# Performance work log

Hardware: AMD Instinct MI355X
Metric: run time of the kernel (lower is better)

Reference implementation:

```python
import jax, jax.numpy as jnp
import numpy as np

N_NODES = 50000


def gcn_conv(x, W, b, src, dst, n):
    # PyG GCNConv: linear transform, add self-loops, symmetric normalization,
    # scatter-add aggregation from src -> dst, then bias.
    h = x @ W  # [N, out]
    loop = jnp.arange(n, dtype=src.dtype)
    s = jnp.concatenate([src, loop])
    d = jnp.concatenate([dst, loop])
    deg = jax.ops.segment_sum(jnp.ones(s.shape[0], dtype=h.dtype), d, num_segments=n)
    dinv = jnp.where(deg > 0, jax.lax.rsqrt(deg), 0.0)
    norm = dinv[s] * dinv[d]  # [E+N]
    msg = h[s] * norm[:, None]
    out = jax.ops.segment_sum(msg, d, num_segments=n)
    return out + b


def setup_inputs() -> dict:
    key = jax.random.key(0)
    ks = jax.random.split(key, 10)
    F_in, H, C = 256, 128, 128
    E, EL = 320000, 200000
    x = jax.random.normal(ks[0], (N_NODES, F_in), dtype=jnp.float32)
    edge_index = jax.random.randint(ks[1], (2, E), 0, N_NODES, dtype=jnp.int32)
    edge_label_index = jax.random.randint(ks[2], (2, EL), 0, N_NODES, dtype=jnp.int32)
    def glorot(k, shape):
        lim = np.sqrt(6.0 / (shape[0] + shape[1]))
        return jax.random.uniform(k, shape, jnp.float32, -lim, lim)
    W0 = glorot(ks[3], (F_in, H))
    b0 = jnp.zeros((H,), jnp.float32)
    W1 = glorot(ks[4], (H, H))
    b1 = jnp.zeros((H,), jnp.float32)
    W2 = glorot(ks[5], (H, C))
    b2 = jnp.zeros((C,), jnp.float32)
    return {"x": x, "edge_index": edge_index, "edge_label_index": edge_label_index,
            "W0": W0, "b0": b0, "W1": W1, "b1": b1, "W2": W2, "b2": b2}


def reference(x, edge_index, edge_label_index, W0, b0, W1, b1, W2, b2):
    src, dst = edge_index[0], edge_index[1]
    n = x.shape[0]
    # drop_edge keep_ratio == 1.0 -> all edges kept (deterministic)
    h = jax.nn.relu(gcn_conv(x, W0, b0, src, dst, n))
    h = jax.nn.relu(gcn_conv(h, W1, b1, src, dst, n))
    z = gcn_conv(h, W2, b2, src, dst, n)  # final conv, no activation
    # decode: dot product over candidate edge pairs
    eli = edge_label_index.astype(jnp.int32)
    logits = jnp.sum(z[eli[0]] * z[eli[1]], axis=-1)  # [E_label]
    return logits
```

## Files before the change

kernel.cpp:

```cpp
#include <hip/hip_runtime.h>
#include <hip/hip_bf16.h>


typedef __attribute__((ext_vector_type(8))) short short8v;
typedef __attribute__((ext_vector_type(4))) float f32x4;

__device__ inline unsigned bf16_rne(float f) {
    unsigned u = __float_as_uint(f);
    return (u + 0x7FFF + ((u >> 16) & 1)) >> 16;
}


__global__ void count_deg_kernel(const int* __restrict__ dst, int* __restrict__ deg, int E) {
    int e = blockIdx.x * blockDim.x + threadIdx.x;
    if (e < E) atomicAdd(&deg[dst[e]], 1);
}

__global__ __launch_bounds__(1024) void scan1_kernel(int* __restrict__ data,
                                                     int* __restrict__ sums, int n) {
    __shared__ int tmp[1024];
    int t = threadIdx.x;
    int idx = blockIdx.x * 1024 + t;
    int val = (idx < n) ? data[idx] : 0;
    tmp[t] = val;
    __syncthreads();
#pragma unroll
    for (int off = 1; off < 1024; off <<= 1) {
        int v = (t >= off) ? tmp[t - off] : 0;
        __syncthreads();
        tmp[t] += v;
        __syncthreads();
    }
    if (idx < n) data[idx] = tmp[t] - val;
    if (t == 1023) sums[blockIdx.x] = tmp[t];
}

__global__ void scan2_kernel(int* __restrict__ sums, int nb) {
    int lane = threadIdx.x & 63;
    int v = (lane < nb) ? sums[lane] : 0;
    int orig = v;
#pragma unroll
    for (int d = 1; d < 64; d <<= 1) {
        int t2 = __shfl_up(v, d, 64);
        if (lane >= d) v += t2;
    }
    if (lane < nb) sums[lane] = v - orig;
}

__global__ __launch_bounds__(1024) void scan3_kernel(int* __restrict__ data,
                                                     const int* __restrict__ sums, int n) {
    int idx = blockIdx.x * 1024 + threadIdx.x;
    if (idx < n && blockIdx.x > 0) data[idx] += sums[blockIdx.x];
}

__global__ void make_dinv_kernel(const int* __restrict__ off, float* __restrict__ dinv,
                                 int n, int E) {
    int v = blockIdx.x * blockDim.x + threadIdx.x;
    if (v < n) {
        int o1 = (v + 1 < n) ? off[v + 1] : E;
        float d = (float)(o1 - off[v]) + 1.0f;
        dinv[v] = 1.0f / sqrtf(d);
    }
}

__global__ void csr_fill_kernel(const int* __restrict__ src, const int* __restrict__ dst,
                                const int* __restrict__ off, int* __restrict__ fill,
                                int* __restrict__ csr_src, int E) {
    int e = blockIdx.x * blockDim.x + threadIdx.x;
    if (e >= E) return;
    int d = dst[e];
    int pos = atomicAdd(&fill[d], 1);
    csr_src[off[d] + pos] = src[e];
}


__global__ void split_w_kernel(const float* __restrict__ W, short* __restrict__ Whp,
                               short* __restrict__ Wlp, int K) {
    int idx = blockIdx.x * blockDim.x + threadIdx.x;
    if (idx >= K * 128) return;
    int k = idx >> 7, col = idx & 127;
    float f = W[idx];
    unsigned h = bf16_rne(f);
    float fh = __uint_as_float(h << 16);
    unsigned l = bf16_rne(f - fh);
    int NS = K >> 5;
    int c = col >> 4, col16 = col & 15, s = k >> 5, q = (k >> 3) & 3, j = k & 7;
    int waddr = (c * NS + s) * 512 + q * 128 + col16 * 8 + j;
    Whp[waddr] = (short)h;
    Wlp[waddr] = (short)l;
}


template<int K>
__global__ __launch_bounds__(256) void pack_a_kernel(const float* __restrict__ x,
                                                     short* __restrict__ Ahp,
                                                     short* __restrict__ Alp,
                                                     int M, int ntiles) {
    int gid = blockIdx.x * blockDim.x + threadIdx.x;
    const int CH = K / 8;
    if (gid >= ntiles * 16 * CH) return;
    int r  = gid & 15;
    int c8 = (gid >> 4) % CH;
    int g  = gid / (16 * CH);
    int row = g * 16 + r;
    if (row >= M) row = M - 1;
    const float* xp = x + (size_t)row * K + c8 * 8;
    float4 v0 = *reinterpret_cast<const float4*>(xp);
    float4 v1 = *reinterpret_cast<const float4*>(xp + 4);
    float f[8] = {v0.x, v0.y, v0.z, v0.w, v1.x, v1.y, v1.z, v1.w};
    short8v hv, lv;
#pragma unroll
    for (int j = 0; j < 8; ++j) {
        unsigned h = bf16_rne(f[j]);
        float fh = __uint_as_float(h << 16);
        unsigned l = bf16_rne(f[j] - fh);
        hv[j] = (short)h;
        lv[j] = (short)l;
    }
    size_t waddr = (size_t)g * 16 * K + c8 * 128 + r * 8;
    *reinterpret_cast<short8v*>(&Ahp[waddr]) = hv;
    *reinterpret_cast<short8v*>(&Alp[waddr]) = lv;
}


template<int K>
__global__ __launch_bounds__(256) void gemm_mfma_packed(const short* __restrict__ Ahp,
                                                        const short* __restrict__ Alp,
                                                        const short* __restrict__ Whp,
                                                        const short* __restrict__ Wlp,
                                                        const float* __restrict__ dinv,
                                                        float* __restrict__ out,
                                                        int M) {
    constexpr int NS = K / 32;
    const int lane = threadIdx.x & 63;
    const int w = threadIdx.x >> 6;
    const int gtile = blockIdx.x * 4 + w;
    const int row16 = gtile * 16;
    if (row16 >= M) return;

    const short* ab = Ahp + (size_t)gtile * 16 * K + lane * 8;
    const short* lb = Alp + (size_t)gtile * 16 * K + lane * 8;

    short8v ah[NS], al[NS];
#pragma unroll
    for (int s = 0; s < NS; ++s) {
        ah[s] = *reinterpret_cast<const short8v*>(ab + s * 512);
        al[s] = *reinterpret_cast<const short8v*>(lb + s * 512);
    }

    f32x4 acc[8];
#pragma unroll
    for (int c = 0; c < 8; ++c) acc[c] = (f32x4){0.f, 0.f, 0.f, 0.f};

#pragma unroll
    for (int c = 0; c < 8; ++c) {
        const short* bb = Whp + (size_t)(c * NS) * 512 + lane * 8;
        const short* cb = Wlp + (size_t)(c * NS) * 512 + lane * 8;
#pragma unroll
        for (int s = 0; s < NS; ++s) {
            short8v bh = *reinterpret_cast<const short8v*>(bb + s * 512);
            short8v bl = *reinterpret_cast<const short8v*>(cb + s * 512);
            acc[c] = __builtin_amdgcn_mfma_f32_16x16x32_bf16(ah[s], bh, acc[c], 0, 0, 0);
            acc[c] = __builtin_amdgcn_mfma_f32_16x16x32_bf16(ah[s], bl, acc[c], 0, 0, 0);
            acc[c] = __builtin_amdgcn_mfma_f32_16x16x32_bf16(al[s], bh, acc[c], 0, 0, 0);
        }
    }

#pragma unroll
    for (int r = 0; r < 4; ++r) {
        int row = row16 + (lane >> 4) * 4 + r;
        if (row < M) {
            float ds = dinv[row];
#pragma unroll
            for (int c = 0; c < 8; ++c)
                out[(size_t)row * 128 + c * 16 + (lane & 15)] = acc[c][r] * ds;
        }
    }
}


template<int PACKED>
__global__ __launch_bounds__(256) void gather_kernel(const int* __restrict__ off,
                                                     const int* __restrict__ csr_src,
                                                     const float* __restrict__ dinv,
                                                     const float* __restrict__ hp,
                                                     const float* __restrict__ bias,
                                                     float* __restrict__ outf,
                                                     short* __restrict__ Ahp,
                                                     short* __restrict__ Alp,
                                                     int n, int E, int do_relu) {
    int gid = blockIdx.x * blockDim.x + threadIdx.x;
    int v = gid >> 6;
    int lane = gid & 63;
    if (v >= n) return;

    int o0 = off[v];
    int o1 = (v + 1 < n) ? off[v + 1] : E;

    const float2* __restrict__ hp2 = reinterpret_cast<const float2*>(hp);
    float2 sv = hp2[(size_t)v * 64 + lane];
    float ax = sv.x, ay = sv.y;
    float bx = 0.0f, by = 0.0f;

    for (int base = o0; base < o1; base += 64) {
        int cnt = min(64, o1 - base);
        int myidx = (lane < cnt) ? csr_src[base + lane] : 0;
        int j = 0;
        for (; j + 4 <= cnt; j += 4) {
            int i0 = __shfl(myidx, j,     64);
            int i1 = __shfl(myidx, j + 1, 64);
            int i2 = __shfl(myidx, j + 2, 64);
            int i3 = __shfl(myidx, j + 3, 64);
            float2 h0 = hp2[(size_t)i0 * 64 + lane];
            float2 h1 = hp2[(size_t)i1 * 64 + lane];
            float2 h2 = hp2[(size_t)i2 * 64 + lane];
            float2 h3 = hp2[(size_t)i3 * 64 + lane];
            ax += h0.x; ay += h0.y;
            bx += h1.x; by += h1.y;
            ax += h2.x; ay += h2.y;
            bx += h3.x; by += h3.y;
        }
        for (; j < cnt; ++j) {
            int s = __shfl(myidx, j, 64);
            float2 hv = hp2[(size_t)s * 64 + lane];
            ax += hv.x; ay += hv.y;
        }
    }

    float dv = dinv[v];
    float2 bb = *reinterpret_cast<const float2*>(&bias[lane * 2]);
    float ox = dv * (ax + bx) + bb.x;
    float oy = dv * (ay + by) + bb.y;
    if (do_relu) { ox = fmaxf(ox, 0.0f); oy = fmaxf(oy, 0.0f); }

    if (PACKED) {
        unsigned h0 = bf16_rne(ox);
        unsigned l0 = bf16_rne(ox - __uint_as_float(h0 << 16));
        unsigned h1 = bf16_rne(oy);
        unsigned l1 = bf16_rne(oy - __uint_as_float(h1 << 16));
        int g = v >> 4, r = v & 15;
        int c8 = lane >> 2;
        int j0 = (2 * lane) & 7;
        size_t a = (size_t)g * 2048 + c8 * 128 + r * 8 + j0;
        short2 hv = make_short2((short)h0, (short)h1);
        short2 lv = make_short2((short)l0, (short)l1);
        *reinterpret_cast<short2*>(&Ahp[a]) = hv;
        *reinterpret_cast<short2*>(&Alp[a]) = lv;
    } else {
        *reinterpret_cast<float2*>(&outf[(size_t)v * 128 + lane * 2]) = make_float2(ox, oy);
    }
}


__global__ __launch_bounds__(256) void decode_kernel(const int* __restrict__ ia,
                                                     const int* __restrict__ ib,
                                                     const float* __restrict__ z,
                                                     float* __restrict__ out, int EL) {
    int gid = blockIdx.x * blockDim.x + threadIdx.x;
    int e = gid >> 5;
    int l5 = gid & 31;
    if (e >= EL) return;
    int a = ia[e], b = ib[e];
    const float4* z4 = reinterpret_cast<const float4*>(z);
    float4 za = z4[(size_t)a * 32 + l5];
    float4 zb = z4[(size_t)b * 32 + l5];
    float s = za.x * zb.x + za.y * zb.y + za.z * zb.z + za.w * zb.w;
#pragma unroll
    for (int off = 16; off > 0; off >>= 1) s += __shfl_down(s, off, 64);
    if (l5 == 0) out[e] = s;
}


extern "C" void kernel_launch(void* const* d_in, const int* in_sizes, int n_in,
                              void* d_out, int out_size, void* d_ws, size_t ws_size,
                              hipStream_t stream) {
    const float* x   = (const float*)d_in[0];
    const int*   ei  = (const int*)d_in[1];
    const int*   eli = (const int*)d_in[2];
    const float* W0  = (const float*)d_in[3];
    const float* b0  = (const float*)d_in[4];
    const float* W1  = (const float*)d_in[5];
    const float* b1  = (const float*)d_in[6];
    const float* W2  = (const float*)d_in[7];
    const float* b2  = (const float*)d_in[8];
    float* out = (float*)d_out;

    const int H    = in_sizes[4];
    const int F_in = in_sizes[3] / H;
    const int n    = in_sizes[0] / F_in;
    const int E    = in_sizes[1] / 2;
    const int EL   = in_sizes[2] / 2;

    const int* src = ei;
    const int* dst = ei + E;
    const int* la  = eli;
    const int* lb  = eli + EL;

    const int ntiles = (n + 15) / 16;

    char* ws = (char*)d_ws;
    size_t p = 0;
    auto alloc = [&](size_t bytes) { char* r = ws + p; p = (p + bytes + 255) & ~(size_t)255; return r; };
    float* dinv    = (float*)alloc((size_t)n * 4);
    int*   off     = (int*)  alloc((size_t)n * 4);
    int*   csr_src = (int*)  alloc((size_t)E * 4);
    int*   sums    = (int*)  alloc(64 * 4);
    short* W0h     = (short*)alloc((size_t)F_in * H * 2);
    short* W0l     = (short*)alloc((size_t)F_in * H * 2);
    short* W1h     = (short*)alloc((size_t)H * H * 2);
    short* W1l     = (short*)alloc((size_t)H * H * 2);
    short* W2h     = (short*)alloc((size_t)H * H * 2);
    short* W2l     = (short*)alloc((size_t)H * H * 2);
    short* pkh     = (short*)alloc((size_t)ntiles * 16 * F_in * 2);
    short* pkl     = (short*)alloc((size_t)ntiles * 16 * F_in * 2);
    float* bufA    = (float*)alloc((size_t)n * 128 * 4);
    float* bufB    = (float*)alloc((size_t)n * 128 * 4);
    int*   fill    = (int*)bufB;

    const int T = 256;
    dim3 blk(T);

    hipMemsetAsync(off, 0, (size_t)n * 4, stream);
    hipMemsetAsync(fill, 0, (size_t)n * 4, stream);
    split_w_kernel<<<(F_in * H + T - 1) / T, blk, 0, stream>>>(W0, W0h, W0l, F_in);
    split_w_kernel<<<(H * H + T - 1) / T, blk, 0, stream>>>(W1, W1h, W1l, H);
    split_w_kernel<<<(H * H + T - 1) / T, blk, 0, stream>>>(W2, W2h, W2l, H);
    {
        long long tot = (long long)ntiles * 16 * (F_in / 8);
        pack_a_kernel<256><<<(int)((tot + T - 1) / T), blk, 0, stream>>>(x, pkh, pkl, n, ntiles);
    }
    count_deg_kernel<<<(E + T - 1) / T, blk, 0, stream>>>(dst, off, E);
    int nb = (n + 1023) / 1024;
    scan1_kernel<<<nb, 1024, 0, stream>>>(off, sums, n);
    scan2_kernel<<<1, 64, 0, stream>>>(sums, nb);
    scan3_kernel<<<nb, 1024, 0, stream>>>(off, sums, n);
    make_dinv_kernel<<<(n + T - 1) / T, blk, 0, stream>>>(off, dinv, n, E);
    csr_fill_kernel<<<(E + T - 1) / T, blk, 0, stream>>>(src, dst, off, fill, csr_src, E);

    const int mblocks       = (ntiles + 3) / 4;
    const int gather_blocks = (int)(((long long)n * 64 + T - 1) / T);

    gemm_mfma_packed<256><<<mblocks, blk, 0, stream>>>(pkh, pkl, W0h, W0l, dinv, bufA, n);
    gather_kernel<1><<<gather_blocks, blk, 0, stream>>>(off, csr_src, dinv, bufA, b0,
                                                        nullptr, pkh, pkl, n, E, 1);

    gemm_mfma_packed<128><<<mblocks, blk, 0, stream>>>(pkh, pkl, W1h, W1l, dinv, bufA, n);
    gather_kernel<1><<<gather_blocks, blk, 0, stream>>>(off, csr_src, dinv, bufA, b1,
                                                        nullptr, pkh, pkl, n, E, 1);

    gemm_mfma_packed<128><<<mblocks, blk, 0, stream>>>(pkh, pkl, W2h, W2l, dinv, bufA, n);
    gather_kernel<0><<<gather_blocks, blk, 0, stream>>>(off, csr_src, dinv, bufA, b2,
                                                        bufB, nullptr, nullptr, n, E, 0);

    const int dec_blocks = (int)(((long long)EL * 32 + T - 1) / T);
    decode_kernel<<<dec_blocks, blk, 0, stream>>>(la, lb, bufB, out, EL);
}
```

Before: 338.1 us.

## Merge weight-split launches, unroll gather by eight, use 512-thread gather blocks

The three weight split-and-pack launches are merged into one kernel that selects the weight matrix by thread index, removing two launches. The gather kernel now runs 512-thread blocks holding 8 nodes each and adds an 8-way unrolled neighbor loop so more independent row loads are in flight. Average degree is about 7, so the 8-way path runs only for higher-degree nodes. Larger blocks may change occupancy and register use.

```diff
diff --git a/kernel.cpp b/kernel.cpp
--- a/kernel.cpp
+++ b/kernel.cpp
@@ -74,10 +74,8 @@
 }
 
 
-__global__ void split_w_kernel(const float* __restrict__ W, short* __restrict__ Whp,
-                               short* __restrict__ Wlp, int K) {
-    int idx = blockIdx.x * blockDim.x + threadIdx.x;
-    if (idx >= K * 128) return;
+__device__ inline void split_pack_one(const float* W, short* Whp, short* Wlp,
+                                      int idx, int K) {
     int k = idx >> 7, col = idx & 127;
     float f = W[idx];
     unsigned h = bf16_rne(f);
@@ -88,6 +86,21 @@
     int waddr = (c * NS + s) * 512 + q * 128 + col16 * 8 + j;
     Whp[waddr] = (short)h;
     Wlp[waddr] = (short)l;
+}
+
+__global__ void split_w_all_kernel(const float* __restrict__ W0, short* __restrict__ W0h,
+                                   short* __restrict__ W0l,
+                                   const float* __restrict__ W1, short* __restrict__ W1h,
+                                   short* __restrict__ W1l,
+                                   const float* __restrict__ W2, short* __restrict__ W2h,
+                                   short* __restrict__ W2l,
+                                   int n0, int n12, int K0, int K12) {
+    int idx = blockIdx.x * blockDim.x + threadIdx.x;
+    if (idx < n0) { split_pack_one(W0, W0h, W0l, idx, K0); return; }
+    idx -= n0;
+    if (idx < n12) { split_pack_one(W1, W1h, W1l, idx, K12); return; }
+    idx -= n12;
+    if (idx < n12) { split_pack_one(W2, W2h, W2l, idx, K12); }
 }
 
 
@@ -180,7 +193,7 @@
 
 
 template<int PACKED>
-__global__ __launch_bounds__(256) void gather_kernel(const int* __restrict__ off,
+__global__ __launch_bounds__(512) void gather_kernel(const int* __restrict__ off,
                                                      const int* __restrict__ csr_src,
                                                      const float* __restrict__ dinv,
                                                      const float* __restrict__ hp,
@@ -189,9 +202,8 @@
                                                      short* __restrict__ Ahp,
                                                      short* __restrict__ Alp,
                                                      int n, int E, int do_relu) {
-    int gid = blockIdx.x * blockDim.x + threadIdx.x;
-    int v = gid >> 6;
-    int lane = gid & 63;
+    int v = blockIdx.x * 8 + (threadIdx.x >> 6);
+    int lane = threadIdx.x & 63;
     if (v >= n) return;
 
     int o0 = off[v];
@@ -206,6 +218,28 @@
         int cnt = min(64, o1 - base);
         int myidx = (lane < cnt) ? csr_src[base + lane] : 0;
         int j = 0;
+        for (; j + 8 <= cnt; j += 8) {
+            int i0 = __shfl(myidx, j,     64);
+            int i1 = __shfl(myidx, j + 1, 64);
+            int i2 = __shfl(myidx, j + 2, 64);
+            int i3 = __shfl(myidx, j + 3, 64);
+            int i4 = __shfl(myidx, j + 4, 64);
+            int i5 = __shfl(myidx, j + 5, 64);
+            int i6 = __shfl(myidx, j + 6, 64);
+            int i7 = __shfl(myidx, j + 7, 64);
+            float2 h0 = hp2[(size_t)i0 * 64 + lane];
+            float2 h1 = hp2[(size_t)i1 * 64 + lane];
+            float2 h2 = hp2[(size_t)i2 * 64 + lane];
+            float2 h3 = hp2[(size_t)i3 * 64 + lane];
+            float2 h4 = hp2[(size_t)i4 * 64 + lane];
+            float2 h5 = hp2[(size_t)i5 * 64 + lane];
+            float2 h6 = hp2[(size_t)i6 * 64 + lane];
+            float2 h7 = hp2[(size_t)i7 * 64 + lane];
+            ax += h0.x; ay += h0.y;  bx += h1.x; by += h1.y;
+            ax += h2.x; ay += h2.y;  bx += h3.x; by += h3.y;
+            ax += h4.x; ay += h4.y;  bx += h5.x; by += h5.y;
+            ax += h6.x; ay += h6.y;  bx += h7.x; by += h7.y;
+        }
         for (; j + 4 <= cnt; j += 4) {
             int i0 = __shfl(myidx, j,     64);
             int i1 = __shfl(myidx, j + 1, 64);
@@ -215,10 +249,8 @@
             float2 h1 = hp2[(size_t)i1 * 64 + lane];
             float2 h2 = hp2[(size_t)i2 * 64 + lane];
             float2 h3 = hp2[(size_t)i3 * 64 + lane];
-            ax += h0.x; ay += h0.y;
-            bx += h1.x; by += h1.y;
-            ax += h2.x; ay += h2.y;
-            bx += h3.x; by += h3.y;
+            ax += h0.x; ay += h0.y;  bx += h1.x; by += h1.y;
+            ax += h2.x; ay += h2.y;  bx += h3.x; by += h3.y;
         }
         for (; j < cnt; ++j) {
             int s = __shfl(myidx, j, 64);
@@ -242,10 +274,8 @@
         int c8 = lane >> 2;
         int j0 = (2 * lane) & 7;
         size_t a = (size_t)g * 2048 + c8 * 128 + r * 8 + j0;
-        short2 hv = make_short2((short)h0, (short)h1);
-        short2 lv = make_short2((short)l0, (short)l1);
-        *reinterpret_cast<short2*>(&Ahp[a]) = hv;
-        *reinterpret_cast<short2*>(&Alp[a]) = lv;
+        *reinterpret_cast<short2*>(&Ahp[a]) = make_short2((short)h0, (short)h1);
+        *reinterpret_cast<short2*>(&Alp[a]) = make_short2((short)l0, (short)l1);
     } else {
         *reinterpret_cast<float2*>(&outf[(size_t)v * 128 + lane * 2]) = make_float2(ox, oy);
     }
@@ -322,9 +352,12 @@
 
     hipMemsetAsync(off, 0, (size_t)n * 4, stream);
     hipMemsetAsync(fill, 0, (size_t)n * 4, stream);
-    split_w_kernel<<<(F_in * H + T - 1) / T, blk, 0, stream>>>(W0, W0h, W0l, F_in);
-    split_w_kernel<<<(H * H + T - 1) / T, blk, 0, stream>>>(W1, W1h, W1l, H);
-    split_w_kernel<<<(H * H + T - 1) / T, blk, 0, stream>>>(W2, W2h, W2l, H);
+    {
+        int n0 = F_in * H, n12 = H * H;
+        int tot = n0 + 2 * n12;
+        split_w_all_kernel<<<(tot + T - 1) / T, blk, 0, stream>>>(
+            W0, W0h, W0l, W1, W1h, W1l, W2, W2h, W2l, n0, n12, F_in, H);
+    }
     {
         long long tot = (long long)ntiles * 16 * (F_in / 8);
         pack_a_kernel<256><<<(int)((tot + T - 1) / T), blk, 0, stream>>>(x, pkh, pkl, n, ntiles);
@@ -338,18 +371,18 @@
     csr_fill_kernel<<<(E + T - 1) / T, blk, 0, stream>>>(src, dst, off, fill, csr_src, E);
 
     const int mblocks       = (ntiles + 3) / 4;
-    const int gather_blocks = (int)(((long long)n * 64 + T - 1) / T);
+    const int gather_blocks = (n + 7) / 8;
 
     gemm_mfma_packed<256><<<mblocks, blk, 0, stream>>>(pkh, pkl, W0h, W0l, dinv, bufA, n);
-    gather_kernel<1><<<gather_blocks, blk, 0, stream>>>(off, csr_src, dinv, bufA, b0,
+    gather_kernel<1><<<gather_blocks, 512, 0, stream>>>(off, csr_src, dinv, bufA, b0,
                                                         nullptr, pkh, pkl, n, E, 1);
 
     gemm_mfma_packed<128><<<mblocks, blk, 0, stream>>>(pkh, pkl, W1h, W1l, dinv, bufA, n);
-    gather_kernel<1><<<gather_blocks, blk, 0, stream>>>(off, csr_src, dinv, bufA, b1,
+    gather_kernel<1><<<gather_blocks, 512, 0, stream>>>(off, csr_src, dinv, bufA, b1,
                                                         nullptr, pkh, pkl, n, E, 1);
 
     gemm_mfma_packed<128><<<mblocks, blk, 0, stream>>>(pkh, pkl, W2h, W2l, dinv, bufA, n);
-    gather_kernel<0><<<gather_blocks, blk, 0, stream>>>(off, csr_src, dinv, bufA, b2,
+    gather_kernel<0><<<gather_blocks, 512, 0, stream>>>(off, csr_src, dinv, bufA, b2,
                                                         bufB, nullptr, nullptr, n, E, 0);
 
     const int dec_blocks = (int)(((long long)EL * 32 + T - 1) / T);
```

Result: no change. 332.9 us (-1.5%).
